# Kernel tuning notes

Measured on AMD Instinct MI355X. Metric: run time of the kernel, lower is better.

## Reference

```python
import jax, jax.numpy as jnp
import numpy as np

EPS = 1e-7  # tf.keras.backend.epsilon()
ROUTING_ITERS = 3


def setup_inputs() -> dict:
    key = jax.random.key(0)
    k1, k2 = jax.random.split(key)
    B, I, Din = 64, 4096, 8
    N, D = 10, 16
    inputs = jax.random.normal(k1, (B, I, Din), dtype=jnp.float32)
    # glorot_uniform-ish init for W [I, N, Din, D]
    limit = (6.0 / (Din + D)) ** 0.5
    W = jax.random.uniform(k2, (I, N, Din, D), dtype=jnp.float32, minval=-limit, maxval=limit)
    return {"inputs": inputs, "W": W}


def _elementwise_squash(s):
    # Original squashes over axis=-2 of [B,1,N,1,D], a size-1 axis ->
    # the reduce_sum is a no-op and squash becomes elementwise.
    sq = s * s
    scale = sq / (1.0 + sq) / jnp.sqrt(sq + EPS)
    return scale * s


def reference(inputs, W):
    # inputs: [B, I, Din], W: [I, N, Din, D]
    # u_hat[b,i,n,d] = sum_p inputs[b,i,p] * W[i,n,p,d]  (the tile+matmul)
    u_hat = jnp.einsum('bip,inpd->bind', inputs, W)  # [B, I, N, D]
    B, I, N, D = u_hat.shape
    b = jnp.zeros((B, I, N, 1), dtype=u_hat.dtype)
    v = None
    for it in range(ROUTING_ITERS):
        c = jax.nn.softmax(b, axis=2)                 # [B, I, N, 1]
        s = jnp.sum(c * u_hat, axis=1)                # [B, N, D]
        v = _elementwise_squash(s)                    # [B, N, D]
        if it < ROUTING_ITERS - 1:
            # agreement: sum over D -> [B, I, N, 1]
            b = b + jnp.sum(u_hat * v[:, None, :, :], axis=-1, keepdims=True)
    # original: squeeze(v[B,1,N,1,D], axis=1) -> [B, N, 1, D]
    return v[:, :, None, :]
```

## Files before the change

kernel.cpp:

```cpp
#include <hip/hip_runtime.h>
#include <math.h>

#define B_ 64
#define I_ 4096
#define P_ 8
#define N_ 10
#define D_ 16
#define ND_ 160
#define BND_ (B_*ND_)
#define EPS_ 1e-7f

#define IPB_ 8
#define NBLK_ (I_ / IPB_)
#define WTILE_ (N_ * P_ * D_)

template<int CTRL>
__device__ __forceinline__ float dpp_bcast(float v) {
    int r = __builtin_amdgcn_update_dpp(0, __float_as_int(v), CTRL, 0xF, 0xF, true);
    return __int_as_float(r);
}

template<int MODE>
__global__ __launch_bounds__(256, 2)
void digitcaps_pass(const float* __restrict__ x, const float* __restrict__ W,
                    const float* __restrict__ Vc, float* __restrict__ part)
{
    __shared__ float wsh[IPB_ * WTILE_];
    const int t = threadIdx.x;
    const int lane = t & 63;
    const int dh = lane & 1;
    const int np = (lane >> 1) & 1;
    const int bl = lane >> 2;
    const int wv = t >> 6;
    const int b  = wv * 16 + bl;
    const int i0 = blockIdx.x * IPB_;

    {
        const float4* __restrict__ Wg = (const float4*)(W + (size_t)i0 * WTILE_);
        float4* __restrict__ Ws = (float4*)wsh;
#pragma unroll
        for (int c = 0; c < (IPB_ * WTILE_) / (4 * 256); ++c)
            Ws[c * 256 + t] = Wg[c * 256 + t];
    }

    float vc[5][8];
    if (MODE == 1) {
#pragma unroll
        for (int k = 0; k < 5; ++k) {
            const float4* vp = (const float4*)(Vc + (size_t)b * ND_ + (np + 2 * k) * D_ + dh * 8);
            float4 v0 = vp[0], v1 = vp[1];
            vc[k][0]=v0.x; vc[k][1]=v0.y; vc[k][2]=v0.z; vc[k][3]=v0.w;
            vc[k][4]=v1.x; vc[k][5]=v1.y; vc[k][6]=v1.z; vc[k][7]=v1.w;
        }
    }

    float acc[5][8];
#pragma unroll
    for (int k = 0; k < 5; ++k)
#pragma unroll
        for (int d = 0; d < 8; ++d) acc[k][d] = 0.f;

    float xv[P_];
    {
        const float4* xp = (const float4*)(x + ((size_t)b * I_ + i0) * P_);
        float4 a0 = xp[0], a1 = xp[1];
        xv[0]=a0.x; xv[1]=a0.y; xv[2]=a0.z; xv[3]=a0.w;
        xv[4]=a1.x; xv[5]=a1.y; xv[6]=a1.z; xv[7]=a1.w;
    }

    __syncthreads();

#pragma unroll 1
    for (int il = 0; il < IPB_; ++il) {
        const float* __restrict__ Wt = wsh + il * WTILE_ + dh * 8;

        float tv[5][8];
#pragma unroll
        for (int k = 0; k < 5; ++k) {
            const float* __restrict__ Wn = Wt + (np + 2 * k) * (P_ * D_);
#pragma unroll
            for (int d = 0; d < 8; ++d) tv[k][d] = 0.f;
#pragma unroll
            for (int p = 0; p < P_; ++p) {
                const float4* __restrict__ wp = (const float4*)(Wn + p * D_);
                float4 wa = wp[0], wb = wp[1];
                float xp = xv[p];
                tv[k][0] = fmaf(wa.x, xp, tv[k][0]);
                tv[k][1] = fmaf(wa.y, xp, tv[k][1]);
                tv[k][2] = fmaf(wa.z, xp, tv[k][2]);
                tv[k][3] = fmaf(wa.w, xp, tv[k][3]);
                tv[k][4] = fmaf(wb.x, xp, tv[k][4]);
                tv[k][5] = fmaf(wb.y, xp, tv[k][5]);
                tv[k][6] = fmaf(wb.z, xp, tv[k][6]);
                tv[k][7] = fmaf(wb.w, xp, tv[k][7]);
            }
        }

        float xn[P_];
        if (il + 1 < IPB_) {
            const float4* xp = (const float4*)(x + ((size_t)b * I_ + i0 + il + 1) * P_);
            float4 a0 = xp[0], a1 = xp[1];
            xn[0]=a0.x; xn[1]=a0.y; xn[2]=a0.z; xn[3]=a0.w;
            xn[4]=a1.x; xn[5]=a1.y; xn[6]=a1.z; xn[7]=a1.w;
        }

        if (MODE == 0) {
#pragma unroll
            for (int k = 0; k < 5; ++k)
#pragma unroll
                for (int d = 0; d < 8; ++d) acc[k][d] += tv[k][d];
        } else {
            float e[5];
            float m = -1e30f;
#pragma unroll
            for (int k = 0; k < 5; ++k) {
                float l = 0.f;
#pragma unroll
                for (int d = 0; d < 8; ++d) l = fmaf(tv[k][d], vc[k][d], l);
                l += dpp_bcast<0xB1>(l);
                e[k] = l;
                m = fmaxf(m, l);
            }
            m = fmaxf(m, dpp_bcast<0x4E>(m));
            float se = 0.f;
#pragma unroll
            for (int k = 0; k < 5; ++k) { e[k] = __expf(e[k] - m); se += e[k]; }
            se += dpp_bcast<0x4E>(se);
            float inv = 1.f / se;
#pragma unroll
            for (int k = 0; k < 5; ++k) {
                float cn = e[k] * inv;
#pragma unroll
                for (int d = 0; d < 8; ++d)
                    acc[k][d] = fmaf(cn, tv[k][d], acc[k][d]);
            }
        }

        if (il + 1 < IPB_) {
#pragma unroll
            for (int p = 0; p < P_; ++p) xv[p] = xn[p];
        }
    }

    float* __restrict__ po = part + (size_t)blockIdx.x * BND_ + (size_t)b * ND_;
#pragma unroll
    for (int k = 0; k < 5; ++k) {
        float* dst = po + (np + 2 * k) * D_ + dh * 8;
        float4 s0 = {acc[k][0], acc[k][1], acc[k][2], acc[k][3]};
        float4 s1 = {acc[k][4], acc[k][5], acc[k][6], acc[k][7]};
        *(float4*)(dst)     = s0;
        *(float4*)(dst + 4) = s1;
    }
}

__global__ __launch_bounds__(256)
void digitcaps_reduce(const float* __restrict__ part, float scale, int mode,
                      float* __restrict__ Vc, float* __restrict__ out)
{
    __shared__ float sm[4][16];
    const int t = threadIdx.x;
    const int kk = t & 15;
    const int tp = t >> 4;
    const int k = blockIdx.x * 16 + kk;

    float s = 0.f;
    const float* __restrict__ p0 = part + (size_t)tp * BND_ + k;
#pragma unroll 8
    for (int j = 0; j < NBLK_ / 16; ++j)
        s += p0[(size_t)j * 16 * BND_];

    s += __shfl_down(s, 32);
    s += __shfl_down(s, 16);
    if ((t & 63) < 16) sm[t >> 6][kk] = s;
    __syncthreads();

    if (t < 16) {
        float tot = (sm[0][t] + sm[1][t]) + (sm[2][t] + sm[3][t]);
        tot *= scale;
        float sq = tot * tot;
        float v = tot * (sq / ((1.f + sq) * sqrtf(sq + EPS_)));
        int j = blockIdx.x * 16 + t;
        if (mode == 0)      Vc[j] = v;
        else if (mode == 1) Vc[j] += v;
        else                out[j] = v;
    }
}

extern "C" void kernel_launch(void* const* d_in, const int* in_sizes, int n_in,
                              void* d_out, int out_size, void* d_ws, size_t ws_size,
                              hipStream_t stream)
{
    const float* x = (const float*)d_in[0];
    const float* W = (const float*)d_in[1];
    float* out = (float*)d_out;

    float* part = (float*)d_ws;
    float* Vc   = part + (size_t)NBLK_ * BND_;

    dim3 pblk(256), pgrid(NBLK_), rblk(256), rgrid(BND_ / 16);

    for (int pass = 0; pass < 3; ++pass) {
        if (pass == 0)
            digitcaps_pass<0><<<pgrid, pblk, 0, stream>>>(x, W, nullptr, part);
        else
            digitcaps_pass<1><<<pgrid, pblk, 0, stream>>>(x, W, Vc, part);
        digitcaps_reduce<<<rgrid, rblk, 0, stream>>>(part, pass == 0 ? 0.1f : 1.0f,
                                                     pass, Vc, out);
    }
}
```

Baseline: 171.3 us.

## Remap threads to 4 batches x 2 d-values and pad shared W tile

Each lane now computes two d-outputs for four batch rows instead of eight d-outputs for one batch row, so every shared-memory W load is reused across four batches. The W tile in LDS is padded (stride 36 per n, 360 per i) to avoid bank conflicts with the new access pattern. The agreement reduction over d now spans 8 lanes, using more DPP steps, and x loads are replicated four times per lane. This is meant to cut LDS traffic per FMA, at the cost of more registers for x and the accumulators and narrower float2 stores.

```diff
diff --git a/kernel.cpp b/kernel.cpp
--- a/kernel.cpp
+++ b/kernel.cpp
@@ -13,6 +13,8 @@
 #define IPB_ 8
 #define NBLK_ (I_ / IPB_)
 #define WTILE_ (N_ * P_ * D_)
+#define NSTR_ 144
+#define ILSTR_ (N_ * NSTR_)
 
 template<int CTRL>
 __device__ __forceinline__ float dpp_bcast(float v) {
@@ -25,131 +27,147 @@
 void digitcaps_pass(const float* __restrict__ x, const float* __restrict__ W,
                     const float* __restrict__ Vc, float* __restrict__ part)
 {
-    __shared__ float wsh[IPB_ * WTILE_];
+    __shared__ float wsh[IPB_ * ILSTR_];
     const int t = threadIdx.x;
     const int lane = t & 63;
-    const int dh = lane & 1;
-    const int np = (lane >> 1) & 1;
-    const int bl = lane >> 2;
-    const int wv = t >> 6;
-    const int b  = wv * 16 + bl;
-    const int i0 = blockIdx.x * IPB_;
+    const int ds  = lane & 7;
+    const int np  = (lane >> 3) & 1;
+    const int bl2 = lane >> 4;
+    const int wv  = t >> 6;
+    const int bb  = wv * 16 + bl2 * 4;
+    const int i0  = blockIdx.x * IPB_;
 
     {
         const float4* __restrict__ Wg = (const float4*)(W + (size_t)i0 * WTILE_);
         float4* __restrict__ Ws = (float4*)wsh;
 #pragma unroll
-        for (int c = 0; c < (IPB_ * WTILE_) / (4 * 256); ++c)
-            Ws[c * 256 + t] = Wg[c * 256 + t];
-    }
-
-    float vc[5][8];
+        for (int c0 = 0; c0 < (IPB_ * WTILE_) / (4 * 256); ++c0) {
+            int c  = c0 * 256 + t;
+            int il = c / 320;
+            int r  = c - il * 320;
+            int n  = r >> 5;
+            int s  = r & 31;
+            Ws[il * 360 + n * 36 + s] = Wg[c];
+        }
+    }
+
+    float vc[4][5][2];
     if (MODE == 1) {
 #pragma unroll
-        for (int k = 0; k < 5; ++k) {
-            const float4* vp = (const float4*)(Vc + (size_t)b * ND_ + (np + 2 * k) * D_ + dh * 8);
-            float4 v0 = vp[0], v1 = vp[1];
-            vc[k][0]=v0.x; vc[k][1]=v0.y; vc[k][2]=v0.z; vc[k][3]=v0.w;
-            vc[k][4]=v1.x; vc[k][5]=v1.y; vc[k][6]=v1.z; vc[k][7]=v1.w;
-        }
-    }
-
-    float acc[5][8];
-#pragma unroll
-    for (int k = 0; k < 5; ++k)
-#pragma unroll
-        for (int d = 0; d < 8; ++d) acc[k][d] = 0.f;
-
-    float xv[P_];
-    {
-        const float4* xp = (const float4*)(x + ((size_t)b * I_ + i0) * P_);
+        for (int j = 0; j < 4; ++j)
+#pragma unroll
+            for (int k = 0; k < 5; ++k) {
+                const float2* vp = (const float2*)(Vc + (size_t)(bb + j) * ND_
+                                                   + (np + 2 * k) * D_ + 2 * ds);
+                float2 v = *vp;
+                vc[j][k][0] = v.x; vc[j][k][1] = v.y;
+            }
+    }
+
+    float acc[4][5][2];
+#pragma unroll
+    for (int j = 0; j < 4; ++j)
+#pragma unroll
+        for (int k = 0; k < 5; ++k) { acc[j][k][0] = 0.f; acc[j][k][1] = 0.f; }
+
+    float xv[4][P_];
+#pragma unroll
+    for (int j = 0; j < 4; ++j) {
+        const float4* xp = (const float4*)(x + ((size_t)(bb + j) * I_ + i0) * P_);
         float4 a0 = xp[0], a1 = xp[1];
-        xv[0]=a0.x; xv[1]=a0.y; xv[2]=a0.z; xv[3]=a0.w;
-        xv[4]=a1.x; xv[5]=a1.y; xv[6]=a1.z; xv[7]=a1.w;
+        xv[j][0]=a0.x; xv[j][1]=a0.y; xv[j][2]=a0.z; xv[j][3]=a0.w;
+        xv[j][4]=a1.x; xv[j][5]=a1.y; xv[j][6]=a1.z; xv[j][7]=a1.w;
     }
 
     __syncthreads();
 
 #pragma unroll 1
     for (int il = 0; il < IPB_; ++il) {
-        const float* __restrict__ Wt = wsh + il * WTILE_ + dh * 8;
-
-        float tv[5][8];
+        const float* __restrict__ Wb = wsh + il * ILSTR_ + np * NSTR_ + 2 * ds;
+
+        float tv[4][5][2];
 #pragma unroll
         for (int k = 0; k < 5; ++k) {
-            const float* __restrict__ Wn = Wt + (np + 2 * k) * (P_ * D_);
-#pragma unroll
-            for (int d = 0; d < 8; ++d) tv[k][d] = 0.f;
+#pragma unroll
+            for (int j = 0; j < 4; ++j) { tv[j][k][0] = 0.f; tv[j][k][1] = 0.f; }
 #pragma unroll
             for (int p = 0; p < P_; ++p) {
-                const float4* __restrict__ wp = (const float4*)(Wn + p * D_);
-                float4 wa = wp[0], wb = wp[1];
-                float xp = xv[p];
-                tv[k][0] = fmaf(wa.x, xp, tv[k][0]);
-                tv[k][1] = fmaf(wa.y, xp, tv[k][1]);
-                tv[k][2] = fmaf(wa.z, xp, tv[k][2]);
-                tv[k][3] = fmaf(wa.w, xp, tv[k][3]);
-                tv[k][4] = fmaf(wb.x, xp, tv[k][4]);
-                tv[k][5] = fmaf(wb.y, xp, tv[k][5]);
-                tv[k][6] = fmaf(wb.z, xp, tv[k][6]);
-                tv[k][7] = fmaf(wb.w, xp, tv[k][7]);
-            }
-        }
-
-        float xn[P_];
+                float2 w = *(const float2*)(Wb + k * 2 * NSTR_ + p * D_);
+#pragma unroll
+                for (int j = 0; j < 4; ++j) {
+                    tv[j][k][0] = fmaf(w.x, xv[j][p], tv[j][k][0]);
+                    tv[j][k][1] = fmaf(w.y, xv[j][p], tv[j][k][1]);
+                }
+            }
+        }
+
+        float xn[4][P_];
         if (il + 1 < IPB_) {
-            const float4* xp = (const float4*)(x + ((size_t)b * I_ + i0 + il + 1) * P_);
-            float4 a0 = xp[0], a1 = xp[1];
-            xn[0]=a0.x; xn[1]=a0.y; xn[2]=a0.z; xn[3]=a0.w;
-            xn[4]=a1.x; xn[5]=a1.y; xn[6]=a1.z; xn[7]=a1.w;
+#pragma unroll
+            for (int j = 0; j < 4; ++j) {
+                const float4* xp = (const float4*)(x + ((size_t)(bb + j) * I_
+                                                        + i0 + il + 1) * P_);
+                float4 a0 = xp[0], a1 = xp[1];
+                xn[j][0]=a0.x; xn[j][1]=a0.y; xn[j][2]=a0.z; xn[j][3]=a0.w;
+                xn[j][4]=a1.x; xn[j][5]=a1.y; xn[j][6]=a1.z; xn[j][7]=a1.w;
+            }
         }
 
         if (MODE == 0) {
 #pragma unroll
-            for (int k = 0; k < 5; ++k)
-#pragma unroll
-                for (int d = 0; d < 8; ++d) acc[k][d] += tv[k][d];
+            for (int j = 0; j < 4; ++j)
+#pragma unroll
+                for (int k = 0; k < 5; ++k) {
+                    acc[j][k][0] += tv[j][k][0];
+                    acc[j][k][1] += tv[j][k][1];
+                }
         } else {
-            float e[5];
-            float m = -1e30f;
-#pragma unroll
-            for (int k = 0; k < 5; ++k) {
-                float l = 0.f;
-#pragma unroll
-                for (int d = 0; d < 8; ++d) l = fmaf(tv[k][d], vc[k][d], l);
-                l += dpp_bcast<0xB1>(l);
-                e[k] = l;
-                m = fmaxf(m, l);
-            }
-            m = fmaxf(m, dpp_bcast<0x4E>(m));
-            float se = 0.f;
-#pragma unroll
-            for (int k = 0; k < 5; ++k) { e[k] = __expf(e[k] - m); se += e[k]; }
-            se += dpp_bcast<0x4E>(se);
-            float inv = 1.f / se;
-#pragma unroll
-            for (int k = 0; k < 5; ++k) {
-                float cn = e[k] * inv;
-#pragma unroll
-                for (int d = 0; d < 8; ++d)
-                    acc[k][d] = fmaf(cn, tv[k][d], acc[k][d]);
+#pragma unroll
+            for (int j = 0; j < 4; ++j) {
+                float e[5];
+                float m = -1e30f;
+#pragma unroll
+                for (int k = 0; k < 5; ++k) {
+                    float l = fmaf(tv[j][k][1], vc[j][k][1],
+                                   tv[j][k][0] * vc[j][k][0]);
+                    l += dpp_bcast<0xB1>(l);
+                    l += dpp_bcast<0x4E>(l);
+                    l += dpp_bcast<0x141>(l);
+                    e[k] = l;
+                    m = fmaxf(m, l);
+                }
+                m = fmaxf(m, dpp_bcast<0x140>(m));
+                float se = 0.f;
+#pragma unroll
+                for (int k = 0; k < 5; ++k) { e[k] = __expf(e[k] - m); se += e[k]; }
+                se += dpp_bcast<0x140>(se);
+                float inv = 1.f / se;
+#pragma unroll
+                for (int k = 0; k < 5; ++k) {
+                    float cn = e[k] * inv;
+                    acc[j][k][0] = fmaf(cn, tv[j][k][0], acc[j][k][0]);
+                    acc[j][k][1] = fmaf(cn, tv[j][k][1], acc[j][k][1]);
+                }
             }
         }
 
         if (il + 1 < IPB_) {
 #pragma unroll
-            for (int p = 0; p < P_; ++p) xv[p] = xn[p];
-        }
-    }
-
-    float* __restrict__ po = part + (size_t)blockIdx.x * BND_ + (size_t)b * ND_;
-#pragma unroll
-    for (int k = 0; k < 5; ++k) {
-        float* dst = po + (np + 2 * k) * D_ + dh * 8;
-        float4 s0 = {acc[k][0], acc[k][1], acc[k][2], acc[k][3]};
-        float4 s1 = {acc[k][4], acc[k][5], acc[k][6], acc[k][7]};
-        *(float4*)(dst)     = s0;
-        *(float4*)(dst + 4) = s1;
+            for (int j = 0; j < 4; ++j)
+#pragma unroll
+                for (int p = 0; p < P_; ++p) xv[j][p] = xn[j][p];
+        }
+    }
+
+#pragma unroll
+    for (int j = 0; j < 4; ++j) {
+        float* __restrict__ dst = part + (size_t)blockIdx.x * BND_
+                                  + (size_t)(bb + j) * ND_ + np * D_ + 2 * ds;
+#pragma unroll
+        for (int k = 0; k < 5; ++k) {
+            float2 s2; s2.x = acc[j][k][0]; s2.y = acc[j][k][1];
+            *(float2*)(dst + k * 2 * D_) = s2;
+        }
     }
 }
 
```

Measured after the change: 157.0 us. 8.4% less time.
